# Kernel tuning notes

Measured on AMD Instinct MI355X. Metric: run time of the kernel, lower is better.

## Reference

```python
import jax, jax.numpy as jnp
import numpy as np

N = 500000     # total nodes across all sets
DIM = 128      # input feature dim
HID = 128      # hidden_dim (output of key_net/val_net)
KDIM = 128     # key_storage.encoder.input_dim
MID = 128      # build_mlp mid width (midmult=1.0 -> (in+out)/2)
NB = 4096      # n_batches

def mish(x):
    return x * jnp.tanh(jax.nn.softplus(x))

def layernorm(x, g, b):
    mu = jnp.mean(x, axis=-1, keepdims=True)
    var = jnp.var(x, axis=-1, keepdims=True)
    return (x - mu) * jax.lax.rsqrt(var + 1e-5) * g + b

def mlp2(x, W1, b1, g, bn, W2, b2):
    # build_mlp(nlayers=2, layernorm=True, nonlinearity=Mish)
    h = layernorm(x @ W1 + b1, g, bn)
    return mish(h) @ W2 + b2

def seg_softmax(x, batch, n):
    # scatter_softmax over the node axis within each segment, per feature
    m = jax.ops.segment_max(x, batch, num_segments=n)
    e = jnp.exp(x - m[batch])
    d = jax.ops.segment_sum(e, batch, num_segments=n)
    return e / d[batch]

def _init(key, fan_in, shape):
    return jax.random.normal(key, shape, dtype=jnp.float32) / np.sqrt(fan_in)

def setup_inputs():
    key = jax.random.key(0)
    ks = jax.random.split(key, 12)
    return {
        "x": jax.random.normal(ks[0], (N, DIM), dtype=jnp.float32),
        "batch": jnp.sort(jax.random.randint(ks[1], (N,), 0, NB)),
        "n_batches": NB,
        # mapping: Linear(dim -> KDIM)
        "W_map": _init(ks[2], DIM, (DIM, KDIM)), "b_map": jnp.zeros(KDIM, jnp.float32),
        # key_net: KDIM -> MID -> HID
        "kW1": _init(ks[3], KDIM, (KDIM, MID)), "kb1": jnp.zeros(MID, jnp.float32),
        "kg": jnp.ones(MID, jnp.float32), "kbn": jnp.zeros(MID, jnp.float32),
        "kW2": _init(ks[4], MID, (MID, HID)), "kb2": jnp.zeros(HID, jnp.float32),
        # val_net: DIM -> MID -> HID
        "vW1": _init(ks[5], DIM, (DIM, MID)), "vb1": jnp.zeros(MID, jnp.float32),
        "vg": jnp.ones(MID, jnp.float32), "vbn": jnp.zeros(MID, jnp.float32),
        "vW2": _init(ks[6], MID, (MID, HID)), "vb2": jnp.zeros(HID, jnp.float32),
        # inner key_storage encoder params (same structure, on keys)
        "iW_map": _init(ks[7], KDIM, (KDIM, KDIM)), "ib_map": jnp.zeros(KDIM, jnp.float32),
        "ikW1": _init(ks[8], KDIM, (KDIM, MID)), "ikb1": jnp.zeros(MID, jnp.float32),
        "ikg": jnp.ones(MID, jnp.float32), "ikbn": jnp.zeros(MID, jnp.float32),
        "ikW2": _init(ks[9], MID, (MID, HID)), "ikb2": jnp.zeros(HID, jnp.float32),
        "ivW1": _init(ks[10], KDIM, (KDIM, MID)), "ivb1": jnp.zeros(MID, jnp.float32),
        "ivg": jnp.ones(MID, jnp.float32), "ivbn": jnp.zeros(MID, jnp.float32),
        "ivW2": _init(ks[11], MID, (MID, HID)), "ivb2": jnp.zeros(HID, jnp.float32),
    }

def reference(x, batch, n_batches, W_map, b_map, kW1, kb1, kg, kbn, kW2, kb2,
              vW1, vb1, vg, vbn, vW2, vb2, iW_map, ib_map,
              ikW1, ikb1, ikg, ikbn, ikW2, ikb2, ivW1, ivb1, ivg, ivbn, ivW2, ivb2):
    # key0 = mapping(x); keys = scatter_softmax(key0, batch)
    key0 = x @ W_map + b_map                      # [N, KDIM]
    keys = seg_softmax(key0, batch, n_batches)    # [N, KDIM]
    # y = val_net(x) * key_net(keys); z = scatter_sum(y, batch)
    y = mlp2(x, vW1, vb1, vg, vbn, vW2, vb2) * mlp2(keys, kW1, kb1, kg, kbn, kW2, kb2)
    z = jax.ops.segment_sum(y, batch, num_segments=n_batches)   # [NB, HID]
    # keyenc = key_storage.encoder(keys, batch): same encoder math applied to keys
    key0b = keys @ iW_map + ib_map
    keys2 = seg_softmax(key0b, batch, n_batches)
    y2 = mlp2(keys, ivW1, ivb1, ivg, ivbn, ivW2, ivb2) * mlp2(keys2, ikW1, ikb1, ikg, ikbn, ikW2, ikb2)
    keyenc = jax.ops.segment_sum(y2, batch, num_segments=n_batches)  # [NB, HID]
    return (z, keyenc)
```

## Files before the change

kernel.cpp:

```cpp
#include <hip/hip_runtime.h>

typedef _Float16 f16;
typedef _Float16 f16x4 __attribute__((ext_vector_type(4)));
typedef _Float16 f16x8 __attribute__((ext_vector_type(8)));
typedef float f32x4 __attribute__((ext_vector_type(4)));

#define NBATCH 4096
#define RMAX 200

__device__ __forceinline__ f32x4 mfma16(f16x8 a, f16x8 b, f32x4 c) {
  return __builtin_amdgcn_mfma_f32_16x16x32_f16(a, b, c, 0, 0, 0);
}

__device__ __forceinline__ int swz(int r, int c) { return r * 128 + (c ^ ((r & 7) << 3)); }

__global__ void seg_bounds(const int* __restrict__ batch, int N, int NB, int* __restrict__ seg) {
  int s = blockIdx.x * blockDim.x + threadIdx.x;
  if (s > NB) return;
  int lo = 0, hi = N;
  while (lo < hi) { int mid = (lo + hi) >> 1; if (batch[mid] < s) lo = mid + 1; else hi = mid; }
  seg[s] = lo;
}

__global__ void pack_weights(const float* w0, const float* w1, const float* w2, const float* w3,
                             const float* w4, const float* w5, const float* w6, const float* w7,
                             const float* w8, const float* w9, f16* __restrict__ Wp) {
  int idx = blockIdx.x * blockDim.x + threadIdx.x;
  if (idx >= 10 * 16384) return;
  int w = idx >> 14, p = idx & 16383;
  int j = p & 7, lane = (p >> 3) & 63, nt = (p >> 9) & 7, kk = p >> 12;
  int k = kk * 32 + (lane >> 4) * 8 + j;
  int n = nt * 16 + (lane & 15);
  const float* W;
  switch (w) {
    case 0: W = w0; break; case 1: W = w1; break; case 2: W = w2; break;
    case 3: W = w3; break; case 4: W = w4; break; case 5: W = w5; break;
    case 6: W = w6; break; case 7: W = w7; break; case 8: W = w8; break;
    default: W = w9; break;
  }
  Wp[idx] = (f16)W[k * 128 + n];
}

__device__ __forceinline__ void gemm_bias_phase(const f16* S, f16* D, const f16* __restrict__ Wg,
    const float* __restrict__ bias, int rows, int mh, int nq, int lane, int quad, int li) {
  int ntl = (rows + 15) >> 4;
  f16x8 bF[4][2];
#pragma unroll
  for (int kk = 0; kk < 4; ++kk)
#pragma unroll
    for (int j = 0; j < 2; ++j)
      bF[kk][j] = *(const f16x8*)(Wg + (size_t)(((kk * 8 + nq * 2 + j) * 64 + lane) * 8));
  float bc[2];
#pragma unroll
  for (int j = 0; j < 2; ++j) bc[j] = bias[(nq * 2 + j) * 16 + li];
  for (int t = mh; t < ntl; t += 2) {
    int m0 = t * 16;
    f32x4 acc0 = {0.f, 0.f, 0.f, 0.f}, acc1 = {0.f, 0.f, 0.f, 0.f};
    int rl = m0 + li;
    bool ok = rl < rows;
#pragma unroll
    for (int kk = 0; kk < 4; ++kk) {
      f16x8 aF = {};
      if (ok) aF = *(const f16x8*)(S + swz(rl, kk * 32 + quad * 8));
      acc0 = mfma16(aF, bF[kk][0], acc0);
      acc1 = mfma16(aF, bF[kk][1], acc1);
    }
#pragma unroll
    for (int r = 0; r < 4; ++r) {
      int row = m0 + quad * 4 + r;
      if (row < rows) {
        D[swz(row, (nq * 2) * 16 + li)] = (f16)(acc0[r] + bc[0]);
        D[swz(row, (nq * 2 + 1) * 16 + li)] = (f16)(acc1[r] + bc[1]);
      }
    }
  }
}

__device__ __forceinline__ void ln_mish_pass(f16* D, const float* __restrict__ g,
                                             const float* __restrict__ bn, int rows, int tid) {
  int part = tid & 3;
  float gv[32], bv[32];
#pragma unroll
  for (int j = 0; j < 8; ++j) {
    float4 gg = *(const float4*)(g + part * 32 + j * 4);
    float4 bb = *(const float4*)(bn + part * 32 + j * 4);
    gv[j * 4 + 0] = gg.x; gv[j * 4 + 1] = gg.y; gv[j * 4 + 2] = gg.z; gv[j * 4 + 3] = gg.w;
    bv[j * 4 + 0] = bb.x; bv[j * 4 + 1] = bb.y; bv[j * 4 + 2] = bb.z; bv[j * 4 + 3] = bb.w;
  }
  for (int r = tid >> 2; r < rows; r += 128) {
    f16x8 v[4];
    float s1 = 0.f, s2 = 0.f;
#pragma unroll
    for (int j = 0; j < 4; ++j) {
      v[j] = *(const f16x8*)(D + swz(r, part * 32 + j * 8));
#pragma unroll
      for (int e = 0; e < 8; ++e) { float f = (float)v[j][e]; s1 += f; s2 += f * f; }
    }
    s1 += __shfl_xor(s1, 1, 64); s2 += __shfl_xor(s2, 1, 64);
    s1 += __shfl_xor(s1, 2, 64); s2 += __shfl_xor(s2, 2, 64);
    float mean = s1 * (1.f / 128.f);
    float var = s2 * (1.f / 128.f) - mean * mean;
    float rstd = rsqrtf(var + 1e-5f);
#pragma unroll
    for (int j = 0; j < 4; ++j) {
      f16x8 o;
#pragma unroll
      for (int e = 0; e < 8; ++e) {
        float u = ((float)v[j][e] - mean) * rstd * gv[j * 8 + e] + bv[j * 8 + e];
        float t = __expf(u);
        float w = t * t + 2.f * t;
        float res = (u > 20.f) ? u : u * (w / (w + 2.f));
        o[e] = (f16)res;
      }
      *(f16x8*)(D + swz(r, part * 32 + j * 8)) = o;
    }
  }
}

__device__ __forceinline__ void softmax_phase(f16* P, int rows, int tid, float* sm, float* sd) {
  int c = tid & 127, st = tid >> 7;
  float m = -3.4e38f, d = 0.f;
#pragma unroll 4
  for (int r = st; r < rows; r += 4) {
    float v = (float)P[swz(r, c)];
    if (v > m) { d = d * __expf(m - v) + 1.f; m = v; } else d += __expf(v - m);
  }
  sm[st * 128 + c] = m; sd[st * 128 + c] = d;
  __syncthreads();
  if (tid < 128) {
    float M = sm[tid], D = sd[tid];
#pragma unroll
    for (int k = 1; k < 4; ++k) {
      float mk = sm[k * 128 + tid], dk = sd[k * 128 + tid];
      if (mk > M) { D = D * __expf(M - mk) + dk; M = mk; } else D += dk * __expf(mk - M);
    }
    sm[tid] = M; sd[tid] = (D > 0.f) ? 1.f / D : 0.f;
  }
  __syncthreads();
  float M = sm[c], inv = sd[c];
#pragma unroll 4
  for (int r = st; r < rows; r += 4)
    P[swz(r, c)] = (f16)(__expf((float)P[swz(r, c)] - M) * inv);
  __syncthreads();
}

__device__ __forceinline__ void pairsum_phase(const f16* S1, const f16* __restrict__ W1,
    const float* __restrict__ b1, const f16* S2, const f16* __restrict__ W2,
    const float* __restrict__ b2, float* __restrict__ outp, int s, int rows,
    int mh, int nq, int lane, int quad, int li, float* red, int tid) {
  f16x8 bF1[4][2], bF2[4][2];
#pragma unroll
  for (int kk = 0; kk < 4; ++kk)
#pragma unroll
    for (int j = 0; j < 2; ++j) {
      size_t off = (size_t)(((kk * 8 + nq * 2 + j) * 64 + lane) * 8);
      bF1[kk][j] = *(const f16x8*)(W1 + off);
      bF2[kk][j] = *(const f16x8*)(W2 + off);
    }
  float b1c[2], b2c[2];
#pragma unroll
  for (int j = 0; j < 2; ++j) {
    b1c[j] = b1[(nq * 2 + j) * 16 + li];
    b2c[j] = b2[(nq * 2 + j) * 16 + li];
  }
  float zs0 = 0.f, zs1 = 0.f;
  int ntl = (rows + 15) >> 4;
  for (int t = mh; t < ntl; t += 2) {
    int m0 = t * 16;
    f32x4 a10 = {0.f,0.f,0.f,0.f}, a11 = {0.f,0.f,0.f,0.f};
    f32x4 a20 = {0.f,0.f,0.f,0.f}, a21 = {0.f,0.f,0.f,0.f};
    int rl = m0 + li;
    bool ok = rl < rows;
#pragma unroll
    for (int kk = 0; kk < 4; ++kk) {
      f16x8 aF1 = {}, aF2 = {};
      if (ok) {
        aF1 = *(const f16x8*)(S1 + swz(rl, kk * 32 + quad * 8));
        aF2 = *(const f16x8*)(S2 + swz(rl, kk * 32 + quad * 8));
      }
      a10 = mfma16(aF1, bF1[kk][0], a10);
      a11 = mfma16(aF1, bF1[kk][1], a11);
      a20 = mfma16(aF2, bF2[kk][0], a20);
      a21 = mfma16(aF2, bF2[kk][1], a21);
    }
    float cs0 = 0.f, cs1 = 0.f;
#pragma unroll
    for (int r = 0; r < 4; ++r) {
      int row = m0 + quad * 4 + r;
      if (row < rows) {
        cs0 += (a10[r] + b1c[0]) * (a20[r] + b2c[0]);
        cs1 += (a11[r] + b1c[1]) * (a21[r] + b2c[1]);
      }
    }
    cs0 += __shfl_xor(cs0, 16, 64); cs0 += __shfl_xor(cs0, 32, 64);
    cs1 += __shfl_xor(cs1, 16, 64); cs1 += __shfl_xor(cs1, 32, 64);
    zs0 += cs0; zs1 += cs1;
  }
  red[tid] = 0.f; red[tid + 512] = 0.f;
  __syncthreads();
  if (quad == 0) {
    int w = tid >> 6;
    red[w * 128 + (nq * 2) * 16 + li] = zs0;
    red[w * 128 + (nq * 2 + 1) * 16 + li] = zs1;
  }
  __syncthreads();
  if (tid < 128) {
    float ssum = 0.f;
#pragma unroll
    for (int w = 0; w < 8; ++w) ssum += red[w * 128 + tid];
    outp[(size_t)s * 128 + tid] = ssum;
  }
  __syncthreads();
}

__global__ __launch_bounds__(512) void encoder_mega(
    const float* __restrict__ x, const int* __restrict__ seg, const f16* __restrict__ Wp,
    const float* b_map, const float* kb1, const float* kg, const float* kbn, const float* kb2,
    const float* vb1, const float* vg, const float* vbn, const float* vb2,
    const float* ib_map, const float* ikb1, const float* ikg, const float* ikbn,
    const float* ikb2, const float* ivb1, const float* ivg, const float* ivbn,
    const float* ivb2, float* __restrict__ Z, float* __restrict__ KE) {
  __shared__ f16 L0[RMAX * 128];
  __shared__ f16 L1[RMAX * 128];
  __shared__ f16 L2[RMAX * 128];
  __shared__ float red[8 * 128];
  __shared__ float sm[512];
  __shared__ float sd[512];
  int s = blockIdx.x;
  int a = seg[s], e = seg[s + 1];
  int rows = e - a;
  int tid = threadIdx.x;
  if (rows <= 0) {
    if (tid < 128) {
      Z[(size_t)s * 128 + tid] = 0.f;
      KE[(size_t)s * 128 + tid] = 0.f;
    }
    return;
  }
  if (rows > RMAX) rows = RMAX;
  int lane = tid & 63, wave = tid >> 6, quad = lane >> 4, li = lane & 15;
  int mh = wave & 1, nq = wave >> 1;

  const float* xa = x + (size_t)a * 128;
  for (int i = tid * 4; i < rows * 128; i += 2048) {
    float4 v = *(const float4*)(xa + i);
    f16x4 h;
    h[0] = (f16)v.x; h[1] = (f16)v.y; h[2] = (f16)v.z; h[3] = (f16)v.w;
    *(f16x4*)(L0 + swz(i >> 7, i & 127)) = h;
  }
  __syncthreads();
  gemm_bias_phase(L0, L1, Wp + 0 * 16384, b_map, rows, mh, nq, lane, quad, li);
  __syncthreads();
  softmax_phase(L1, rows, tid, sm, sd);
  gemm_bias_phase(L0, L2, Wp + 3 * 16384, vb1, rows, mh, nq, lane, quad, li);
  __syncthreads();
  ln_mish_pass(L2, vg, vbn, rows, tid);
  __syncthreads();
  gemm_bias_phase(L1, L0, Wp + 1 * 16384, kb1, rows, mh, nq, lane, quad, li);
  __syncthreads();
  ln_mish_pass(L0, kg, kbn, rows, tid);
  __syncthreads();
  pairsum_phase(L2, Wp + 4 * 16384, vb2, L0, Wp + 2 * 16384, kb2, Z, s, rows,
                mh, nq, lane, quad, li, red, tid);
  gemm_bias_phase(L1, L2, Wp + 5 * 16384, ib_map, rows, mh, nq, lane, quad, li);
  __syncthreads();
  softmax_phase(L2, rows, tid, sm, sd);
  gemm_bias_phase(L1, L0, Wp + 8 * 16384, ivb1, rows, mh, nq, lane, quad, li);
  __syncthreads();
  ln_mish_pass(L0, ivg, ivbn, rows, tid);
  __syncthreads();
  gemm_bias_phase(L2, L1, Wp + 6 * 16384, ikb1, rows, mh, nq, lane, quad, li);
  __syncthreads();
  ln_mish_pass(L1, ikg, ikbn, rows, tid);
  __syncthreads();
  pairsum_phase(L0, Wp + 9 * 16384, ivb2, L1, Wp + 7 * 16384, ikb2, KE, s, rows,
                mh, nq, lane, quad, li, red, tid);
}

extern "C" void kernel_launch(void* const* d_in, const int* in_sizes, int n_in,
                              void* d_out, int out_size, void* d_ws, size_t ws_size,
                              hipStream_t stream) {
  const float* x = (const float*)d_in[0];
  const int* batch = (const int*)d_in[1];
  const int N = in_sizes[1];
  const float* W_map = (const float*)d_in[3];  const float* b_map = (const float*)d_in[4];
  const float* kW1 = (const float*)d_in[5];    const float* kb1 = (const float*)d_in[6];
  const float* kg = (const float*)d_in[7];     const float* kbn = (const float*)d_in[8];
  const float* kW2 = (const float*)d_in[9];    const float* kb2 = (const float*)d_in[10];
  const float* vW1 = (const float*)d_in[11];   const float* vb1 = (const float*)d_in[12];
  const float* vg = (const float*)d_in[13];    const float* vbn = (const float*)d_in[14];
  const float* vW2 = (const float*)d_in[15];   const float* vb2 = (const float*)d_in[16];
  const float* iW_map = (const float*)d_in[17];const float* ib_map = (const float*)d_in[18];
  const float* ikW1 = (const float*)d_in[19];  const float* ikb1 = (const float*)d_in[20];
  const float* ikg = (const float*)d_in[21];   const float* ikbn = (const float*)d_in[22];
  const float* ikW2 = (const float*)d_in[23];  const float* ikb2 = (const float*)d_in[24];
  const float* ivW1 = (const float*)d_in[25];  const float* ivb1 = (const float*)d_in[26];
  const float* ivg = (const float*)d_in[27];   const float* ivbn = (const float*)d_in[28];
  const float* ivW2 = (const float*)d_in[29];  const float* ivb2 = (const float*)d_in[30];

  char* ws = (char*)d_ws;
  int* seg = (int*)ws;
  f16* Wp = (f16*)(ws + 32768);

  float* Z = (float*)d_out;
  float* KE = Z + (out_size / 2);

  seg_bounds<<<(NBATCH + 1 + 255) / 256, 256, 0, stream>>>(batch, N, NBATCH, seg);
  pack_weights<<<(10 * 16384) / 256, 256, 0, stream>>>(
      W_map, kW1, kW2, vW1, vW2, iW_map, ikW1, ikW2, ivW1, ivW2, Wp);

  encoder_mega<<<NBATCH, 512, 0, stream>>>(
      x, seg, Wp, b_map, kb1, kg, kbn, kb2, vb1, vg, vbn, vb2,
      ib_map, ikb1, ikg, ikbn, ikb2, ivb1, ivg, ivbn, ivb2, Z, KE);
}
```

Baseline: 1.289 ms.

## Double block size to 1024 threads and rewrite softmax as register-resident two-pass

Launches the fused encoder kernel with 1024 threads per segment instead of 512. GEMM row tiles are now split across 4 wave groups instead of 2, and LayerNorm/Mish uses 8 threads per row. The segmented softmax is rewritten so each thread holds up to four rows of 8 columns in registers, computes max and sum with shuffles plus shared-memory partials, and writes results back directly, replacing the per-column online-softmax loops. This raises parallelism and cuts shared-memory traffic in softmax. In exchange, rows beyond 256 would be silently dropped in softmax (RMAX is 200, so this is safe), and register pressure under 1024-thread launch bounds may limit occupancy.

```diff
diff --git a/kernel.cpp b/kernel.cpp
--- a/kernel.cpp
+++ b/kernel.cpp
@@ -42,7 +42,7 @@
 }
 
 __device__ __forceinline__ void gemm_bias_phase(const f16* S, f16* D, const f16* __restrict__ Wg,
-    const float* __restrict__ bias, int rows, int mh, int nq, int lane, int quad, int li) {
+    const float* __restrict__ bias, int rows, int mq, int nq, int lane, int quad, int li) {
   int ntl = (rows + 15) >> 4;
   f16x8 bF[4][2];
 #pragma unroll
@@ -53,7 +53,7 @@
   float bc[2];
 #pragma unroll
   for (int j = 0; j < 2; ++j) bc[j] = bias[(nq * 2 + j) * 16 + li];
-  for (int t = mh; t < ntl; t += 2) {
+  for (int t = mq; t < ntl; t += 4) {
     int m0 = t * 16;
     f32x4 acc0 = {0.f, 0.f, 0.f, 0.f}, acc1 = {0.f, 0.f, 0.f, 0.f};
     int rl = m0 + li;
@@ -78,76 +78,147 @@
 
 __device__ __forceinline__ void ln_mish_pass(f16* D, const float* __restrict__ g,
                                              const float* __restrict__ bn, int rows, int tid) {
-  int part = tid & 3;
-  float gv[32], bv[32];
-#pragma unroll
-  for (int j = 0; j < 8; ++j) {
-    float4 gg = *(const float4*)(g + part * 32 + j * 4);
-    float4 bb = *(const float4*)(bn + part * 32 + j * 4);
+  int part = tid & 7;
+  int cbase = part * 16;
+  float gv[16], bv[16];
+#pragma unroll
+  for (int j = 0; j < 4; ++j) {
+    float4 gg = *(const float4*)(g + cbase + j * 4);
+    float4 bb = *(const float4*)(bn + cbase + j * 4);
     gv[j * 4 + 0] = gg.x; gv[j * 4 + 1] = gg.y; gv[j * 4 + 2] = gg.z; gv[j * 4 + 3] = gg.w;
     bv[j * 4 + 0] = bb.x; bv[j * 4 + 1] = bb.y; bv[j * 4 + 2] = bb.z; bv[j * 4 + 3] = bb.w;
   }
-  for (int r = tid >> 2; r < rows; r += 128) {
-    f16x8 v[4];
+  for (int r = tid >> 3; r < rows; r += 128) {
+    f16x8 v0 = *(const f16x8*)(D + swz(r, cbase));
+    f16x8 v1 = *(const f16x8*)(D + swz(r, cbase + 8));
+    float f[16];
+#pragma unroll
+    for (int e = 0; e < 8; ++e) { f[e] = (float)v0[e]; f[8 + e] = (float)v1[e]; }
     float s1 = 0.f, s2 = 0.f;
 #pragma unroll
-    for (int j = 0; j < 4; ++j) {
-      v[j] = *(const f16x8*)(D + swz(r, part * 32 + j * 8));
-#pragma unroll
-      for (int e = 0; e < 8; ++e) { float f = (float)v[j][e]; s1 += f; s2 += f * f; }
-    }
+    for (int e = 0; e < 16; ++e) { s1 += f[e]; s2 = fmaf(f[e], f[e], s2); }
     s1 += __shfl_xor(s1, 1, 64); s2 += __shfl_xor(s2, 1, 64);
     s1 += __shfl_xor(s1, 2, 64); s2 += __shfl_xor(s2, 2, 64);
+    s1 += __shfl_xor(s1, 4, 64); s2 += __shfl_xor(s2, 4, 64);
     float mean = s1 * (1.f / 128.f);
     float var = s2 * (1.f / 128.f) - mean * mean;
     float rstd = rsqrtf(var + 1e-5f);
-#pragma unroll
-    for (int j = 0; j < 4; ++j) {
-      f16x8 o;
-#pragma unroll
-      for (int e = 0; e < 8; ++e) {
-        float u = ((float)v[j][e] - mean) * rstd * gv[j * 8 + e] + bv[j * 8 + e];
-        float t = __expf(u);
-        float w = t * t + 2.f * t;
-        float res = (u > 20.f) ? u : u * (w / (w + 2.f));
-        o[e] = (f16)res;
-      }
-      *(f16x8*)(D + swz(r, part * 32 + j * 8)) = o;
-    }
-  }
-}
-
-__device__ __forceinline__ void softmax_phase(f16* P, int rows, int tid, float* sm, float* sd) {
-  int c = tid & 127, st = tid >> 7;
-  float m = -3.4e38f, d = 0.f;
-#pragma unroll 4
-  for (int r = st; r < rows; r += 4) {
-    float v = (float)P[swz(r, c)];
-    if (v > m) { d = d * __expf(m - v) + 1.f; m = v; } else d += __expf(v - m);
-  }
-  sm[st * 128 + c] = m; sd[st * 128 + c] = d;
+    float mr = -mean * rstd;
+    f16x8 o0, o1;
+#pragma unroll
+    for (int e = 0; e < 16; ++e) {
+      float u = fmaf(fmaf(f[e], rstd, mr), gv[e], bv[e]);
+      float t = __expf(u);
+      float w = t * t + 2.f * t;
+      float res = (u > 20.f) ? u : u * (w / (w + 2.f));
+      if (e < 8) o0[e] = (f16)res; else o1[e - 8] = (f16)res;
+    }
+    *(f16x8*)(D + swz(r, cbase)) = o0;
+    *(f16x8*)(D + swz(r, cbase + 8)) = o1;
+  }
+}
+
+__device__ __forceinline__ void softmax_phase(f16* P, int rows, int tid,
+                                              float* __restrict__ pm, float* __restrict__ mbuf) {
+  int cg = tid & 15, st = tid >> 4;
+  int c8 = cg * 8;
+  int wv = tid >> 6;
+  f16x8 NEGV;
+#pragma unroll
+  for (int e = 0; e < 8; ++e) NEGV[e] = (f16)(-65504.f);
+  int r0 = st, r1 = st + 64, r2 = st + 128, r3 = st + 192;
+  f16x8 v0 = (r0 < rows) ? *(const f16x8*)(P + swz(r0, c8)) : NEGV;
+  f16x8 v1 = (r1 < rows) ? *(const f16x8*)(P + swz(r1, c8)) : NEGV;
+  f16x8 v2 = (r2 < rows) ? *(const f16x8*)(P + swz(r2, c8)) : NEGV;
+  f16x8 v3 = (r3 < rows) ? *(const f16x8*)(P + swz(r3, c8)) : NEGV;
+  float m8[8];
+#pragma unroll
+  for (int e = 0; e < 8; ++e) {
+    float a = (float)v0[e], b = (float)v1[e], c = (float)v2[e], d = (float)v3[e];
+    m8[e] = fmaxf(fmaxf(a, b), fmaxf(c, d));
+    m8[e] = fmaxf(m8[e], __shfl_xor(m8[e], 16, 64));
+    m8[e] = fmaxf(m8[e], __shfl_xor(m8[e], 32, 64));
+  }
+  if ((tid & 63) < 16) {
+    float4 pa = {m8[0], m8[1], m8[2], m8[3]}, pb = {m8[4], m8[5], m8[6], m8[7]};
+    *(float4*)(pm + wv * 128 + c8) = pa;
+    *(float4*)(pm + wv * 128 + c8 + 4) = pb;
+  }
   __syncthreads();
   if (tid < 128) {
-    float M = sm[tid], D = sd[tid];
-#pragma unroll
-    for (int k = 1; k < 4; ++k) {
-      float mk = sm[k * 128 + tid], dk = sd[k * 128 + tid];
-      if (mk > M) { D = D * __expf(M - mk) + dk; M = mk; } else D += dk * __expf(mk - M);
-    }
-    sm[tid] = M; sd[tid] = (D > 0.f) ? 1.f / D : 0.f;
-  }
-  __syncthreads();
-  float M = sm[c], inv = sd[c];
-#pragma unroll 4
-  for (int r = st; r < rows; r += 4)
-    P[swz(r, c)] = (f16)(__expf((float)P[swz(r, c)] - M) * inv);
-  __syncthreads();
+    float M = pm[tid];
+#pragma unroll
+    for (int w = 1; w < 16; ++w) M = fmaxf(M, pm[w * 128 + tid]);
+    mbuf[tid] = M;
+  }
+  __syncthreads();
+  float M8[8];
+  {
+    float4 a = *(const float4*)(mbuf + c8);
+    float4 b = *(const float4*)(mbuf + c8 + 4);
+    M8[0] = a.x; M8[1] = a.y; M8[2] = a.z; M8[3] = a.w;
+    M8[4] = b.x; M8[5] = b.y; M8[6] = b.z; M8[7] = b.w;
+  }
+  float d8[8];
+#pragma unroll
+  for (int e = 0; e < 8; ++e) {
+    float s = __expf((float)v0[e] - M8[e]) + __expf((float)v1[e] - M8[e]) +
+              __expf((float)v2[e] - M8[e]) + __expf((float)v3[e] - M8[e]);
+    s += __shfl_xor(s, 16, 64);
+    s += __shfl_xor(s, 32, 64);
+    d8[e] = s;
+  }
+  __syncthreads();
+  if ((tid & 63) < 16) {
+    float4 pa = {d8[0], d8[1], d8[2], d8[3]}, pb = {d8[4], d8[5], d8[6], d8[7]};
+    *(float4*)(pm + wv * 128 + c8) = pa;
+    *(float4*)(pm + wv * 128 + c8 + 4) = pb;
+  }
+  __syncthreads();
+  if (tid < 128) {
+    float Dv = 0.f;
+#pragma unroll
+    for (int w = 0; w < 16; ++w) Dv += pm[w * 128 + tid];
+    mbuf[tid] = (Dv > 0.f) ? 1.f / Dv : 0.f;
+  }
+  __syncthreads();
+  float I8[8];
+  {
+    float4 a = *(const float4*)(mbuf + c8);
+    float4 b = *(const float4*)(mbuf + c8 + 4);
+    I8[0] = a.x; I8[1] = a.y; I8[2] = a.z; I8[3] = a.w;
+    I8[4] = b.x; I8[5] = b.y; I8[6] = b.z; I8[7] = b.w;
+  }
+  if (r0 < rows) {
+    f16x8 o;
+#pragma unroll
+    for (int e = 0; e < 8; ++e) o[e] = (f16)(__expf((float)v0[e] - M8[e]) * I8[e]);
+    *(f16x8*)(P + swz(r0, c8)) = o;
+  }
+  if (r1 < rows) {
+    f16x8 o;
+#pragma unroll
+    for (int e = 0; e < 8; ++e) o[e] = (f16)(__expf((float)v1[e] - M8[e]) * I8[e]);
+    *(f16x8*)(P + swz(r1, c8)) = o;
+  }
+  if (r2 < rows) {
+    f16x8 o;
+#pragma unroll
+    for (int e = 0; e < 8; ++e) o[e] = (f16)(__expf((float)v2[e] - M8[e]) * I8[e]);
+    *(f16x8*)(P + swz(r2, c8)) = o;
+  }
+  if (r3 < rows) {
+    f16x8 o;
+#pragma unroll
+    for (int e = 0; e < 8; ++e) o[e] = (f16)(__expf((float)v3[e] - M8[e]) * I8[e]);
+    *(f16x8*)(P + swz(r3, c8)) = o;
+  }
 }
 
 __device__ __forceinline__ void pairsum_phase(const f16* S1, const f16* __restrict__ W1,
     const float* __restrict__ b1, const f16* S2, const f16* __restrict__ W2,
     const float* __restrict__ b2, float* __restrict__ outp, int s, int rows,
-    int mh, int nq, int lane, int quad, int li, float* red, int tid) {
+    int mq, int nq, int lane, int quad, int li, float* red, int tid) {
   f16x8 bF1[4][2], bF2[4][2];
 #pragma unroll
   for (int kk = 0; kk < 4; ++kk)
@@ -165,7 +236,7 @@
   }
   float zs0 = 0.f, zs1 = 0.f;
   int ntl = (rows + 15) >> 4;
-  for (int t = mh; t < ntl; t += 2) {
+  for (int t = mq; t < ntl; t += 4) {
     int m0 = t * 16;
     f32x4 a10 = {0.f,0.f,0.f,0.f}, a11 = {0.f,0.f,0.f,0.f};
     f32x4 a20 = {0.f,0.f,0.f,0.f}, a21 = {0.f,0.f,0.f,0.f};
@@ -196,24 +267,19 @@
     cs1 += __shfl_xor(cs1, 16, 64); cs1 += __shfl_xor(cs1, 32, 64);
     zs0 += cs0; zs1 += cs1;
   }
-  red[tid] = 0.f; red[tid + 512] = 0.f;
-  __syncthreads();
   if (quad == 0) {
-    int w = tid >> 6;
-    red[w * 128 + (nq * 2) * 16 + li] = zs0;
-    red[w * 128 + (nq * 2 + 1) * 16 + li] = zs1;
+    red[mq * 128 + nq * 32 + li] = zs0;
+    red[mq * 128 + nq * 32 + 16 + li] = zs1;
   }
   __syncthreads();
   if (tid < 128) {
-    float ssum = 0.f;
-#pragma unroll
-    for (int w = 0; w < 8; ++w) ssum += red[w * 128 + tid];
+    float ssum = red[tid] + red[128 + tid] + red[256 + tid] + red[384 + tid];
     outp[(size_t)s * 128 + tid] = ssum;
   }
   __syncthreads();
 }
 
-__global__ __launch_bounds__(512) void encoder_mega(
+__global__ __launch_bounds__(1024) void encoder_mega(
     const float* __restrict__ x, const int* __restrict__ seg, const f16* __restrict__ Wp,
     const float* b_map, const float* kb1, const float* kg, const float* kbn, const float* kb2,
     const float* vb1, const float* vg, const float* vbn, const float* vb2,
@@ -223,9 +289,8 @@
   __shared__ f16 L0[RMAX * 128];
   __shared__ f16 L1[RMAX * 128];
   __shared__ f16 L2[RMAX * 128];
-  __shared__ float red[8 * 128];
-  __shared__ float sm[512];
-  __shared__ float sd[512];
+  __shared__ float pm[16 * 128];
+  __shared__ float mbuf[128];
   int s = blockIdx.x;
   int a = seg[s], e = seg[s + 1];
   int rows = e - a;
@@ -239,42 +304,44 @@
   }
   if (rows > RMAX) rows = RMAX;
   int lane = tid & 63, wave = tid >> 6, quad = lane >> 4, li = lane & 15;
-  int mh = wave & 1, nq = wave >> 1;
+  int mq = wave & 3, nq = wave >> 2;
 
   const float* xa = x + (size_t)a * 128;
-  for (int i = tid * 4; i < rows * 128; i += 2048) {
-    float4 v = *(const float4*)(xa + i);
-    f16x4 h;
-    h[0] = (f16)v.x; h[1] = (f16)v.y; h[2] = (f16)v.z; h[3] = (f16)v.w;
-    *(f16x4*)(L0 + swz(i >> 7, i & 127)) = h;
-  }
-  __syncthreads();
-  gemm_bias_phase(L0, L1, Wp + 0 * 16384, b_map, rows, mh, nq, lane, quad, li);
-  __syncthreads();
-  softmax_phase(L1, rows, tid, sm, sd);
-  gemm_bias_phase(L0, L2, Wp + 3 * 16384, vb1, rows, mh, nq, lane, quad, li);
+  for (int i = tid * 8; i < rows * 128; i += 8192) {
+    float4 u0 = *(const float4*)(xa + i);
+    float4 u1 = *(const float4*)(xa + i + 4);
+    f16x8 h;
+    h[0] = (f16)u0.x; h[1] = (f16)u0.y; h[2] = (f16)u0.z; h[3] = (f16)u0.w;
+    h[4] = (f16)u1.x; h[5] = (f16)u1.y; h[6] = (f16)u1.z; h[7] = (f16)u1.w;
+    *(f16x8*)(L0 + swz(i >> 7, i & 127)) = h;
+  }
+  __syncthreads();
+  gemm_bias_phase(L0, L1, Wp + 0 * 16384, b_map, rows, mq, nq, lane, quad, li);
+  __syncthreads();
+  softmax_phase(L1, rows, tid, pm, mbuf);
+  gemm_bias_phase(L0, L2, Wp + 3 * 16384, vb1, rows, mq, nq, lane, quad, li);
   __syncthreads();
   ln_mish_pass(L2, vg, vbn, rows, tid);
   __syncthreads();
-  gemm_bias_phase(L1, L0, Wp + 1 * 16384, kb1, rows, mh, nq, lane, quad, li);
+  gemm_bias_phase(L1, L0, Wp + 1 * 16384, kb1, rows, mq, nq, lane, quad, li);
   __syncthreads();
   ln_mish_pass(L0, kg, kbn, rows, tid);
   __syncthreads();
   pairsum_phase(L2, Wp + 4 * 16384, vb2, L0, Wp + 2 * 16384, kb2, Z, s, rows,
-                mh, nq, lane, quad, li, red, tid);
-  gemm_bias_phase(L1, L2, Wp + 5 * 16384, ib_map, rows, mh, nq, lane, quad, li);
-  __syncthreads();
-  softmax_phase(L2, rows, tid, sm, sd);
-  gemm_bias_phase(L1, L0, Wp + 8 * 16384, ivb1, rows, mh, nq, lane, quad, li);
+                mq, nq, lane, quad, li, pm, tid);
+  gemm_bias_phase(L1, L2, Wp + 5 * 16384, ib_map, rows, mq, nq, lane, quad, li);
+  __syncthreads();
+  softmax_phase(L2, rows, tid, pm, mbuf);
+  gemm_bias_phase(L1, L0, Wp + 8 * 16384, ivb1, rows, mq, nq, lane, quad, li);
   __syncthreads();
   ln_mish_pass(L0, ivg, ivbn, rows, tid);
   __syncthreads();
-  gemm_bias_phase(L2, L1, Wp + 6 * 16384, ikb1, rows, mh, nq, lane, quad, li);
+  gemm_bias_phase(L2, L1, Wp + 6 * 16384, ikb1, rows, mq, nq, lane, quad, li);
   __syncthreads();
   ln_mish_pass(L1, ikg, ikbn, rows, tid);
   __syncthreads();
   pairsum_phase(L0, Wp + 9 * 16384, ivb2, L1, Wp + 7 * 16384, ikb2, KE, s, rows,
-                mh, nq, lane, quad, li, red, tid);
+                mq, nq, lane, quad, li, pm, tid);
 }
 
 extern "C" void kernel_launch(void* const* d_in, const int* in_sizes, int n_in,
@@ -309,7 +376,7 @@
   pack_weights<<<(10 * 16384) / 256, 256, 0, stream>>>(
       W_map, kW1, kW2, vW1, vW2, iW_map, ikW1, ikW2, ivW1, ivW2, Wp);
 
-  encoder_mega<<<NBATCH, 512, 0, stream>>>(
+  encoder_mega<<<NBATCH, 1024, 0, stream>>>(
       x, seg, Wp, b_map, kb1, kg, kbn, kb2, vb1, vg, vbn, vb2,
       ib_map, ikb1, ikg, ikbn, ikb2, ivb1, ivg, ivbn, ivb2, Z, KE);
 }
```

Result: faster. 1.105 ms (-14.3%).
